# Kernel optimization log

Hardware: AMD Instinct MI355X
Metric: run time of the kernel (lower is better)

Reference implementation:

```python
import jax, jax.numpy as jnp
import numpy as np

B, S, D, H = 8, 1024, 768, 12
DH = D // H
EPS = 1e-5


def setup_inputs() -> dict:
    key = jax.random.key(0)
    ks = jax.random.split(key, 12)
    sc_h = 1.0 / np.sqrt(DH)
    sc_d = 1.0 / np.sqrt(D)
    return {
        "x": jax.random.normal(ks[0], (B, S, D), jnp.float32),
        "ln1_g": jnp.ones((D,), jnp.float32),
        "ln1_b": jnp.zeros((D,), jnp.float32),
        "Wq": jax.random.normal(ks[1], (H, DH, DH), jnp.float32) * sc_h,
        "bq": jax.random.normal(ks[2], (H, DH), jnp.float32) * 0.01,
        "Wk": jax.random.normal(ks[3], (H, DH, DH), jnp.float32) * sc_h,
        "bk": jax.random.normal(ks[4], (H, DH), jnp.float32) * 0.01,
        "Wv": jax.random.normal(ks[5], (H, DH, DH), jnp.float32) * sc_h,
        "bv": jax.random.normal(ks[6], (H, DH), jnp.float32) * 0.01,
        "ln2_g": jnp.ones((D,), jnp.float32),
        "ln2_b": jnp.zeros((D,), jnp.float32),
        "W1": jax.random.normal(ks[7], (D, 4 * D), jnp.float32) * sc_d,  # c_fc (bias=False)
        "W2": jax.random.normal(ks[8], (4 * D, D), jnp.float32) * (1.0 / np.sqrt(4 * D)),  # c_proj (bias=False)
    }


def _layernorm(x, g, b):
    m = jnp.mean(x, axis=-1, keepdims=True)
    v = jnp.mean(jnp.square(x - m), axis=-1, keepdims=True)
    return (x - m) * jax.lax.rsqrt(v + EPS) * g + b


def _msa(x, Wq, bq, Wk, bk, Wv, bv):
    b, s, d = x.shape
    h = x.reshape(b, s, H, DH)  # per-head slices of the embedding
    q = jnp.einsum('bshd,hde->bhse', h, Wq) + bq[None, :, None, :]
    k = jnp.einsum('bshd,hde->bhse', h, Wk) + bk[None, :, None, :]
    v = jnp.einsum('bshd,hde->bhse', h, Wv) + bv[None, :, None, :]
    scores = jnp.einsum('bhse,bhte->bhst', q, k) / np.sqrt(DH).astype(np.float32)
    attn = jax.nn.softmax(scores, axis=-1)
    o = jnp.einsum('bhst,bhte->bhse', attn, v)
    return o.transpose(0, 2, 1, 3).reshape(b, s, d)  # concat heads


def reference(x, ln1_g, ln1_b, Wq, bq, Wk, bk, Wv, bv, ln2_g, ln2_b, W1, W2):
    out = x + _msa(_layernorm(x, ln1_g, ln1_b), Wq, bq, Wk, bk, Wv, bv)
    h = _layernorm(out, ln2_g, ln2_b)
    ffn = jnp.dot(jax.nn.gelu(jnp.dot(h, W1), approximate=False), W2)
    return out + ffn
```

## Files before the change

kernel.cpp:

```cpp
#include <hip/hip_runtime.h>
#include <hip/hip_bf16.h>
#include <math.h>

#define B_ 8
#define S_ 1024
#define D_ 768
#define H_ 12
#define QSCALE 0.18033688011112042f

typedef __attribute__((ext_vector_type(8))) short short8;
typedef __attribute__((ext_vector_type(4))) float floatx4;
typedef unsigned short ushort_t;

__device__ __forceinline__ ushort_t f2bf(float f) {
  unsigned int u = __builtin_bit_cast(unsigned int, f);
  u += 0x7fffu + ((u >> 16) & 1u);
  return (ushort_t)(u >> 16);
}

__device__ __forceinline__ unsigned int pkbf(float a, float b) {
  __hip_bfloat162 h = __float22bfloat162_rn(make_float2(a, b));
  unsigned int r;
  __builtin_memcpy(&r, &h, sizeof(r));
  return r;
}

__device__ __forceinline__ float gelu_f(float x) {
  const float z = fabsf(x) * 0.70710678118654752f;
  const float t = __builtin_amdgcn_rcpf(1.0f + 0.3275911f * z);
  const float p =
      t * (0.254829592f +
           t * (-0.284496736f +
                t * (1.421413741f + t * (-1.453152027f + t * 1.061405429f))));
  const float e = __expf(-z * z);
  const float erfv = 1.0f - p * e;
  return 0.5f * x * (1.0f + copysignf(erfv, x));
}

template <int N>
__device__ __forceinline__ void wait_vmcnt() {
  if constexpr (N == 0)
    asm volatile("s_waitcnt vmcnt(0)" ::: "memory");
  else if constexpr (N == 6)
    asm volatile("s_waitcnt vmcnt(6)" ::: "memory");
  else
    asm volatile("s_waitcnt vmcnt(8)" ::: "memory");
}

__global__ __launch_bounds__(256) void ln_bf16(
    const float* __restrict__ in, const float* __restrict__ g,
    const float* __restrict__ bias, ushort_t* __restrict__ out) {
  const int row = blockIdx.x * 4 + (threadIdx.x >> 6);
  const int lane = threadIdx.x & 63;
  const float* p = in + (size_t)row * D_;
  float4 v[3];
#pragma unroll
  for (int j = 0; j < 3; ++j) v[j] = *(const float4*)(p + j * 256 + lane * 4);
  float s = 0.f;
#pragma unroll
  for (int j = 0; j < 3; ++j) s += (v[j].x + v[j].y) + (v[j].z + v[j].w);
#pragma unroll
  for (int m = 1; m < 64; m <<= 1) s += __shfl_xor(s, m);
  const float mean = s * (1.0f / D_);
  float q = 0.f;
#pragma unroll
  for (int j = 0; j < 3; ++j) {
    const float a = v[j].x - mean, b = v[j].y - mean;
    const float c = v[j].z - mean, d = v[j].w - mean;
    q += (a * a + b * b) + (c * c + d * d);
  }
#pragma unroll
  for (int m = 1; m < 64; m <<= 1) q += __shfl_xor(q, m);
  const float rstd = rsqrtf(q * (1.0f / D_) + 1e-5f);
  ushort_t* o = out + (size_t)row * D_;
#pragma unroll
  for (int j = 0; j < 3; ++j) {
    const float4 gv = *(const float4*)(g + j * 256 + lane * 4);
    const float4 bv = *(const float4*)(bias + j * 256 + lane * 4);
    const unsigned int p01 = pkbf((v[j].x - mean) * rstd * gv.x + bv.x,
                                  (v[j].y - mean) * rstd * gv.y + bv.y);
    const unsigned int p23 = pkbf((v[j].z - mean) * rstd * gv.z + bv.z,
                                  (v[j].w - mean) * rstd * gv.w + bv.w);
    *(uint2*)(o + j * 256 + lane * 4) = make_uint2(p01, p23);
  }
}

__global__ __launch_bounds__(256) void transpose_cast(
    const float* __restrict__ W, ushort_t* __restrict__ Wt, int Kdim, int Ndim) {
  __shared__ float tile[32][33];
  const int n0 = blockIdx.x * 32, k0 = blockIdx.y * 32;
  const int tx = threadIdx.x & 31, ty = threadIdx.x >> 5;
#pragma unroll
  for (int i = 0; i < 32; i += 8)
    tile[ty + i][tx] = W[(size_t)(k0 + ty + i) * Ndim + n0 + tx];
  __syncthreads();
#pragma unroll
  for (int i = 0; i < 32; i += 8)
    Wt[(size_t)(n0 + ty + i) * Kdim + k0 + tx] = f2bf(tile[tx][ty + i]);
}

__global__ __launch_bounds__(256) void trans_w64(
    const float* __restrict__ Wq, const float* __restrict__ Wk,
    const float* __restrict__ Wv, ushort_t* __restrict__ Wqt,
    ushort_t* __restrict__ Wkt, ushort_t* __restrict__ Wvt) {
  const int h = blockIdx.x;
  const float* W = blockIdx.y == 0 ? Wq : blockIdx.y == 1 ? Wk : Wv;
  ushort_t* O = blockIdx.y == 0 ? Wqt : blockIdx.y == 1 ? Wkt : Wvt;
  __shared__ float t[64][65];
  const int tid = threadIdx.x;
#pragma unroll
  for (int i = 0; i < 16; ++i) {
    const int idx = tid + i * 256;
    t[idx >> 6][idx & 63] = W[h * 4096 + idx];
  }
  __syncthreads();
#pragma unroll
  for (int i = 0; i < 16; ++i) {
    const int idx = tid + i * 256;
    O[h * 4096 + idx] = f2bf(t[idx & 63][idx >> 6]);
  }
}

__global__ __launch_bounds__(256) void qkv_mfma(
    const ushort_t* __restrict__ xbf,
    const ushort_t* __restrict__ Wqt, const ushort_t* __restrict__ Wkt,
    const ushort_t* __restrict__ Wvt,
    const float* __restrict__ bq, const float* __restrict__ bk,
    const float* __restrict__ bv,
    ushort_t* __restrict__ qo, ushort_t* __restrict__ ko,
    ushort_t* __restrict__ vt) {
  const int h = blockIdx.y;
  const int mb = blockIdx.x * 128;
  const int tid = threadIdx.x;
  const int wave = tid >> 6, lane = tid & 63;
  const int lc = lane & 15, kq = lane >> 4;
  const int wm = wave * 32;

  short8 af[2][2];
#pragma unroll
  for (int mi = 0; mi < 2; ++mi)
#pragma unroll
    for (int kc = 0; kc < 2; ++kc)
      af[mi][kc] = *(const short8*)(xbf + (size_t)(mb + wm + mi * 16 + lc) * D_ +
                                    h * 64 + kc * 32 + kq * 8);

  const ushort_t* Wp[3] = {Wqt + h * 4096, Wkt + h * 4096, Wvt + h * 4096};
  floatx4 acc[3][2][4] = {};
#pragma unroll
  for (int w3 = 0; w3 < 3; ++w3)
#pragma unroll
    for (int n = 0; n < 4; ++n)
#pragma unroll
      for (int kc = 0; kc < 2; ++kc) {
        const short8 bfv =
            *(const short8*)(Wp[w3] + (n * 16 + lc) * 64 + kc * 32 + kq * 8);
#pragma unroll
        for (int mi = 0; mi < 2; ++mi)
          acc[w3][mi][n] = __builtin_amdgcn_mfma_f32_16x16x32_bf16(
              af[mi][kc], bfv, acc[w3][mi][n], 0, 0, 0);
      }

  const int b = mb >> 10;
  const size_t obase = (size_t)(b * H_ + h) * (S_ * 64);
#pragma unroll
  for (int w3 = 0; w3 < 2; ++w3) {
    const float* bias = (w3 == 0 ? bq : bk) + h * 64;
    ushort_t* outp = w3 == 0 ? qo : ko;
#pragma unroll
    for (int n = 0; n < 4; ++n) {
      const int e = n * 16 + lc;
      const float bvv = bias[e];
#pragma unroll
      for (int mi = 0; mi < 2; ++mi)
#pragma unroll
        for (int r = 0; r < 4; ++r) {
          const int sl = (mb & 1023) + wm + mi * 16 + kq * 4 + r;
          float v = acc[w3][mi][n][r] + bvv;
          if (w3 == 0) v *= QSCALE;
          outp[obase + (size_t)sl * 64 + e] = f2bf(v);
        }
    }
  }
#pragma unroll
  for (int n = 0; n < 4; ++n) {
    const int e = n * 16 + lc;
    const float bvv = bv[h * 64 + e];
#pragma unroll
    for (int mi = 0; mi < 2; ++mi) {
      const int sl0 = (mb & 1023) + wm + mi * 16 + kq * 4;
      const unsigned int p01 =
          pkbf(acc[2][mi][n][0] + bvv, acc[2][mi][n][1] + bvv);
      const unsigned int p23 =
          pkbf(acc[2][mi][n][2] + bvv, acc[2][mi][n][3] + bvv);
      *(uint2*)(vt + obase + (size_t)e * S_ + sl0) = make_uint2(p01, p23);
    }
  }
}

__global__ __launch_bounds__(256) void attn_mfma(
    const ushort_t* __restrict__ qb, const ushort_t* __restrict__ kb,
    const ushort_t* __restrict__ vt, const float* __restrict__ x,
    float* __restrict__ out1) {
  const int bh = blockIdx.x;
  const int tid = threadIdx.x;
  const int wave = tid >> 6, lane = tid & 63;
  const int lc = lane & 15, kq = lane >> 4;
  const int q0 = blockIdx.y * 128 + wave * 32;

  __shared__ __align__(16) ushort_t Ks[64 * 64];
  __shared__ __align__(16) ushort_t Vs[64 * 64];
  __shared__ __align__(16) ushort_t Pw[4][2][16 * 72];

  const ushort_t* qp = qb + (size_t)bh * (S_ * 64);
  const ushort_t* kp = kb + (size_t)bh * (S_ * 64);
  const ushort_t* vp = vt + (size_t)bh * (S_ * 64);

  short8 qf[2][2];
#pragma unroll
  for (int qi = 0; qi < 2; ++qi)
#pragma unroll
    for (int kc = 0; kc < 2; ++kc)
      qf[qi][kc] = *(const short8*)(qp + (size_t)(q0 + qi * 16 + lc) * 64 +
                                    kc * 32 + kq * 8);

  const int srow = tid >> 3;
  const int sgc = ((tid & 7) ^ (srow & 7)) * 8;
  const int slds = srow * 64 + (tid & 7) * 8;
  const int swz = lc & 7;

  float l_r[2] = {0.0f, 0.0f};
  floatx4 oacc[2][4] = {};

  for (int kt = 0; kt < 16; ++kt) {
#pragma unroll
    for (int half = 0; half < 2; ++half) {
      const int r = half * 32 + srow;
      __builtin_amdgcn_global_load_lds(
          (const __attribute__((address_space(1))) unsigned int*)
              (kp + (size_t)(kt * 64 + r) * 64 + sgc),
          (__attribute__((address_space(3))) unsigned int*)
              (Ks + half * 2048 + slds), 16, 0, 0);
      __builtin_amdgcn_global_load_lds(
          (const __attribute__((address_space(1))) unsigned int*)
              (vp + (size_t)r * S_ + kt * 64 + sgc),
          (__attribute__((address_space(3))) unsigned int*)
              (Vs + half * 2048 + slds), 16, 0, 0);
    }
    __syncthreads();

    floatx4 sacc[2][4] = {};
#pragma unroll
    for (int mi = 0; mi < 4; ++mi) {
      const int row = (mi * 16 + lc) * 64;
#pragma unroll
      for (int kc = 0; kc < 2; ++kc) {
        const short8 kf =
            *(const short8*)(Ks + row + ((kc * 4 + kq) ^ swz) * 8);
        sacc[0][mi] = __builtin_amdgcn_mfma_f32_16x16x32_bf16(
            kf, qf[0][kc], sacc[0][mi], 0, 0, 0);
        sacc[1][mi] = __builtin_amdgcn_mfma_f32_16x16x32_bf16(
            kf, qf[1][kc], sacc[1][mi], 0, 0, 0);
      }
    }

#pragma unroll
    for (int qi = 0; qi < 2; ++qi) {
      float pr[4][4];
      float sm = 0.f;
#pragma unroll
      for (int mi = 0; mi < 4; ++mi)
#pragma unroll
        for (int r = 0; r < 4; ++r) {
          pr[mi][r] = exp2f(sacc[qi][mi][r]);
          sm += pr[mi][r];
        }
      l_r[qi] += sm;
#pragma unroll
      for (int mi = 0; mi < 4; ++mi) {
        const unsigned int p01 = pkbf(pr[mi][0], pr[mi][1]);
        const unsigned int p23 = pkbf(pr[mi][2], pr[mi][3]);
        *(uint2*)(&Pw[wave][qi][lc * 72 + mi * 16 + kq * 4]) =
            make_uint2(p01, p23);
      }
    }
    asm volatile("s_waitcnt lgkmcnt(0)" ::: "memory");

    short8 pf[2][2];
#pragma unroll
    for (int qi = 0; qi < 2; ++qi)
#pragma unroll
      for (int kc = 0; kc < 2; ++kc)
        pf[qi][kc] =
            *(const short8*)(&Pw[wave][qi][lc * 72 + kc * 32 + kq * 8]);
#pragma unroll
    for (int mi = 0; mi < 4; ++mi) {
      const int row = (mi * 16 + lc) * 64;
#pragma unroll
      for (int kc = 0; kc < 2; ++kc) {
        const short8 vf =
            *(const short8*)(Vs + row + ((kc * 4 + kq) ^ swz) * 8);
        oacc[0][mi] = __builtin_amdgcn_mfma_f32_16x16x32_bf16(
            vf, pf[0][kc], oacc[0][mi], 0, 0, 0);
        oacc[1][mi] = __builtin_amdgcn_mfma_f32_16x16x32_bf16(
            vf, pf[1][kc], oacc[1][mi], 0, 0, 0);
      }
    }
    __syncthreads();
  }

  const int b = bh / H_, h = bh % H_;
  float* Ow = (float*)&Pw[wave][0][0];
#pragma unroll
  for (int qi = 0; qi < 2; ++qi) {
    float lt = l_r[qi];
    lt += __shfl_xor(lt, 16);
    lt += __shfl_xor(lt, 32);
    const float inv = 1.0f / lt;
#pragma unroll
    for (int mi = 0; mi < 4; ++mi) {
      floatx4 ov = oacc[qi][mi];
      ov[0] *= inv; ov[1] *= inv; ov[2] *= inv; ov[3] *= inv;
      *(floatx4*)(&Ow[lc * 68 + mi * 16 + kq * 4]) = ov;
    }
    asm volatile("s_waitcnt lgkmcnt(0)" ::: "memory");
    const int row = (lane >> 3) & 7, c8 = (lane & 7) * 4;
#pragma unroll
    for (int rg = 0; rg < 2; ++rg) {
      const int qq = rg * 8 + row;
      const size_t gbase =
          ((size_t)(b * S_) + q0 + qi * 16 + qq) * D_ + h * 64 + c8;
#pragma unroll
      for (int j = 0; j < 2; ++j) {
        const float4 ov = *(const float4*)(&Ow[qq * 68 + j * 32 + c8]);
        const float4 xv = *(const float4*)(x + gbase + j * 32);
        *(float4*)(out1 + gbase + j * 32) =
            make_float4(ov.x + xv.x, ov.y + xv.y, ov.z + xv.z, ov.w + xv.w);
      }
    }
    asm volatile("s_waitcnt lgkmcnt(0)" ::: "memory");
  }
}

template <int BM, int BN, int N, int K, bool GELU, bool RESID, bool OUT_BF16,
          bool XCDMAP>
__global__ __launch_bounds__(256) void gemm_pipe(
    const ushort_t* __restrict__ A, const ushort_t* __restrict__ Bt,
    const float* __restrict__ resid, void* __restrict__ Cout) {
  constexpr int MI = BM / 32;
  constexpr int NJ = BN / 32;
  constexpr int LPT = (BM + BN) / 32;
  constexpr int NT = K / 64;

  int mb, nb;
  if constexpr (XCDMAP) {
    const int lin = blockIdx.x;
    const int xcd = lin & 7, slot = lin >> 3;
    const int mbg = slot / (N / 128), nbi = slot - mbg * (N / 128);
    mb = (xcd * 16 + mbg) * 64;
    nb = nbi * 128;
  } else {
    nb = blockIdx.x * BN;
    mb = blockIdx.y * BM;
  }

  const int tid = threadIdx.x;
  const int wave = tid >> 6, lane = tid & 63;
  const int wm = (wave >> 1) * (BM / 2), wn = (wave & 1) * (BN / 2);

  __shared__ __align__(16) ushort_t Asp[2][BM * 64];
  __shared__ __align__(16) ushort_t Bsp[2][BN * 64];

  const int sr = tid >> 3;
  const int sc8 = (tid & 7) * 8;
  const int sgx = ((tid & 7) ^ (sr & 7)) * 8;

  auto stage = [&](int t, int buf) {
    const int kb = t * 64;
#pragma unroll
    for (int j = 0; j < BM / 32; ++j) {
      const int row = j * 32 + sr;
      __builtin_amdgcn_global_load_lds(
          (const __attribute__((address_space(1))) unsigned int*)
              (A + (size_t)(mb + row) * K + kb + sgx),
          (__attribute__((address_space(3))) unsigned int*)
              (&Asp[buf][row * 64 + sc8]), 16, 0, 0);
    }
#pragma unroll
    for (int j = 0; j < BN / 32; ++j) {
      const int row = j * 32 + sr;
      __builtin_amdgcn_global_load_lds(
          (const __attribute__((address_space(1))) unsigned int*)
              (Bt + (size_t)(nb + row) * K + kb + sgx),
          (__attribute__((address_space(3))) unsigned int*)
              (&Bsp[buf][row * 64 + sc8]), 16, 0, 0);
    }
  };

  stage(0, 0);
  stage(1, 1);
  wait_vmcnt<LPT>();
  __builtin_amdgcn_s_barrier();
  __builtin_amdgcn_sched_barrier(0);

  const int lc = lane & 15, kq = lane >> 4, swz = lc & 7;
  floatx4 acc[MI][NJ] = {};

#pragma unroll 1
  for (int t = 0; t < NT; ++t) {
    const int cur = t & 1;
    short8 af[MI][2], bfr[NJ][2];
#pragma unroll
    for (int i = 0; i < MI; ++i)
#pragma unroll
      for (int ks = 0; ks < 2; ++ks)
        af[i][ks] = *(const short8*)(&Asp[cur][(wm + i * 16 + lc) * 64 +
                                               ((ks * 4 + kq) ^ swz) * 8]);
#pragma unroll
    for (int j = 0; j < NJ; ++j)
#pragma unroll
      for (int ks = 0; ks < 2; ++ks)
        bfr[j][ks] = *(const short8*)(&Bsp[cur][(wn + j * 16 + lc) * 64 +
                                                ((ks * 4 + kq) ^ swz) * 8]);
    asm volatile("s_waitcnt lgkmcnt(0)" ::: "memory");
    __builtin_amdgcn_sched_barrier(0);
    __builtin_amdgcn_s_barrier();
    __builtin_amdgcn_sched_barrier(0);
    if (t + 2 < NT) stage(t + 2, cur);
    __builtin_amdgcn_sched_barrier(0);
    __builtin_amdgcn_s_setprio(1);
#pragma unroll
    for (int ks = 0; ks < 2; ++ks)
#pragma unroll
      for (int i = 0; i < MI; ++i)
#pragma unroll
        for (int j = 0; j < NJ; ++j)
          acc[i][j] = __builtin_amdgcn_mfma_f32_16x16x32_bf16(
              af[i][ks], bfr[j][ks], acc[i][j], 0, 0, 0);
    __builtin_amdgcn_s_setprio(0);
    if (t + 2 < NT)
      wait_vmcnt<LPT>();
    else if (t + 1 < NT)
      wait_vmcnt<0>();
    if (t + 1 < NT) {
      __builtin_amdgcn_s_barrier();
      __builtin_amdgcn_sched_barrier(0);
    }
  }

  const int lcol = lane & 15, lr4 = (lane >> 4) * 4;
#pragma unroll
  for (int i = 0; i < MI; ++i)
#pragma unroll
    for (int r = 0; r < 4; ++r) {
      const int m = mb + wm + i * 16 + lr4 + r;
#pragma unroll
      for (int j = 0; j < NJ; ++j) {
        const int col = nb + wn + j * 16 + lcol;
        float vv = acc[i][j][r];
        if (GELU) vv = gelu_f(vv);
        if (RESID) vv += resid[(size_t)m * N + col];
        if (OUT_BF16)
          ((ushort_t*)Cout)[(size_t)m * N + col] = f2bf(vv);
        else
          ((float*)Cout)[(size_t)m * N + col] = vv;
      }
    }
}

extern "C" void kernel_launch(void* const* d_in, const int* in_sizes, int n_in,
                              void* d_out, int out_size, void* d_ws, size_t ws_size,
                              hipStream_t stream) {
  (void)in_sizes; (void)n_in; (void)out_size; (void)ws_size;
  const float* x     = (const float*)d_in[0];
  const float* ln1_g = (const float*)d_in[1];
  const float* ln1_b = (const float*)d_in[2];
  const float* Wq    = (const float*)d_in[3];
  const float* bq    = (const float*)d_in[4];
  const float* Wk    = (const float*)d_in[5];
  const float* bk    = (const float*)d_in[6];
  const float* Wv    = (const float*)d_in[7];
  const float* bv    = (const float*)d_in[8];
  const float* ln2_g = (const float*)d_in[9];
  const float* ln2_b = (const float*)d_in[10];
  const float* W1    = (const float*)d_in[11];
  const float* W2    = (const float*)d_in[12];
  float* out = (float*)d_out;

  const size_t n = (size_t)B_ * S_ * D_;
  ushort_t* u = (ushort_t*)d_ws;
  ushort_t* xbf  = u;
  ushort_t* qb   = xbf + n;
  ushort_t* kb   = qb + n;
  ushort_t* vt   = kb + n;
  ushort_t* xbf2 = vt + n;
  ushort_t* act  = xbf2 + n;
  ushort_t* Wt1  = act + (size_t)8192 * 3072;
  ushort_t* Wt2  = Wt1 + (size_t)3072 * 768;
  ushort_t* Wqt  = Wt2 + (size_t)768 * 3072;
  ushort_t* Wkt  = Wqt + H_ * 4096;
  ushort_t* Wvt  = Wkt + H_ * 4096;
  float* out1 = (float*)(Wvt + H_ * 4096);

  trans_w64<<<dim3(12, 3), dim3(256), 0, stream>>>(Wq, Wk, Wv, Wqt, Wkt, Wvt);
  transpose_cast<<<dim3(96, 24), dim3(256), 0, stream>>>(W1, Wt1, 768, 3072);
  transpose_cast<<<dim3(24, 96), dim3(256), 0, stream>>>(W2, Wt2, 3072, 768);
  ln_bf16<<<dim3(2048), dim3(256), 0, stream>>>(x, ln1_g, ln1_b, xbf);
  qkv_mfma<<<dim3(64, 12), dim3(256), 0, stream>>>(xbf, Wqt, Wkt, Wvt,
                                                   bq, bk, bv, qb, kb, vt);
  attn_mfma<<<dim3(96, 8), dim3(256), 0, stream>>>(qb, kb, vt, x, out1);
  ln_bf16<<<dim3(2048), dim3(256), 0, stream>>>(out1, ln2_g, ln2_b, xbf2);
  gemm_pipe<128, 128, 3072, 768, true, false, true, false>
      <<<dim3(24, 64), dim3(256), 0, stream>>>(xbf2, Wt1, nullptr, act);
  gemm_pipe<64, 128, 768, 3072, false, true, false, true>
      <<<dim3(768), dim3(256), 0, stream>>>(act, Wt2, out1, out);
}
```

Baseline: 292.9 us.

## Double-buffer K/V tiles in attention kernel to overlap loads with MFMA

The attention kernel now keeps two LDS buffers for K and V and prefetches the next key tile with global_load_lds while the current tile is processed. Partial vmcnt waits and raw s_barrier calls replace the full __syncthreads, so that global load latency can hide behind the QK and PV MFMA work. This doubles the K/V LDS footprint, which may lower occupancy, and depends on the vmcnt count matching the four loads issued per tile.

```diff
diff --git a/kernel.cpp b/kernel.cpp
--- a/kernel.cpp
+++ b/kernel.cpp
@@ -41,6 +41,8 @@
 __device__ __forceinline__ void wait_vmcnt() {
   if constexpr (N == 0)
     asm volatile("s_waitcnt vmcnt(0)" ::: "memory");
+  else if constexpr (N == 4)
+    asm volatile("s_waitcnt vmcnt(4)" ::: "memory");
   else if constexpr (N == 6)
     asm volatile("s_waitcnt vmcnt(6)" ::: "memory");
   else
@@ -207,8 +209,8 @@
   const int lc = lane & 15, kq = lane >> 4;
   const int q0 = blockIdx.y * 128 + wave * 32;
 
-  __shared__ __align__(16) ushort_t Ks[64 * 64];
-  __shared__ __align__(16) ushort_t Vs[64 * 64];
+  __shared__ __align__(16) ushort_t Ks[2][64 * 64];
+  __shared__ __align__(16) ushort_t Vs[2][64 * 64];
   __shared__ __align__(16) ushort_t Pw[4][2][16 * 72];
 
   const ushort_t* qp = qb + (size_t)bh * (S_ * 64);
@@ -228,10 +230,7 @@
   const int slds = srow * 64 + (tid & 7) * 8;
   const int swz = lc & 7;
 
-  float l_r[2] = {0.0f, 0.0f};
-  floatx4 oacc[2][4] = {};
-
-  for (int kt = 0; kt < 16; ++kt) {
+  auto stageKV = [&](int kt, int buf) {
 #pragma unroll
     for (int half = 0; half < 2; ++half) {
       const int r = half * 32 + srow;
@@ -239,14 +238,31 @@
           (const __attribute__((address_space(1))) unsigned int*)
               (kp + (size_t)(kt * 64 + r) * 64 + sgc),
           (__attribute__((address_space(3))) unsigned int*)
-              (Ks + half * 2048 + slds), 16, 0, 0);
+              (&Ks[buf][half * 2048 + slds]), 16, 0, 0);
       __builtin_amdgcn_global_load_lds(
           (const __attribute__((address_space(1))) unsigned int*)
               (vp + (size_t)r * S_ + kt * 64 + sgc),
           (__attribute__((address_space(3))) unsigned int*)
-              (Vs + half * 2048 + slds), 16, 0, 0);
-    }
-    __syncthreads();
+              (&Vs[buf][half * 2048 + slds]), 16, 0, 0);
+    }
+  };
+
+  float l_r[2] = {0.0f, 0.0f};
+  floatx4 oacc[2][4] = {};
+
+  stageKV(0, 0);
+
+#pragma unroll 1
+  for (int kt = 0; kt < 16; ++kt) {
+    const int cur = kt & 1;
+    if (kt + 1 < 16) stageKV(kt + 1, cur ^ 1);
+    if (kt + 1 < 16)
+      wait_vmcnt<4>();
+    else
+      wait_vmcnt<0>();
+    __builtin_amdgcn_sched_barrier(0);
+    __builtin_amdgcn_s_barrier();
+    __builtin_amdgcn_sched_barrier(0);
 
     floatx4 sacc[2][4] = {};
 #pragma unroll
@@ -255,7 +271,7 @@
 #pragma unroll
       for (int kc = 0; kc < 2; ++kc) {
         const short8 kf =
-            *(const short8*)(Ks + row + ((kc * 4 + kq) ^ swz) * 8);
+            *(const short8*)(&Ks[cur][row + ((kc * 4 + kq) ^ swz) * 8]);
         sacc[0][mi] = __builtin_amdgcn_mfma_f32_16x16x32_bf16(
             kf, qf[0][kc], sacc[0][mi], 0, 0, 0);
         sacc[1][mi] = __builtin_amdgcn_mfma_f32_16x16x32_bf16(
@@ -298,14 +314,18 @@
 #pragma unroll
       for (int kc = 0; kc < 2; ++kc) {
         const short8 vf =
-            *(const short8*)(Vs + row + ((kc * 4 + kq) ^ swz) * 8);
+            *(const short8*)(&Vs[cur][row + ((kc * 4 + kq) ^ swz) * 8]);
         oacc[0][mi] = __builtin_amdgcn_mfma_f32_16x16x32_bf16(
             vf, pf[0][kc], oacc[0][mi], 0, 0, 0);
         oacc[1][mi] = __builtin_amdgcn_mfma_f32_16x16x32_bf16(
             vf, pf[1][kc], oacc[1][mi], 0, 0, 0);
       }
     }
-    __syncthreads();
+    if (kt + 1 < 16) {
+      __builtin_amdgcn_sched_barrier(0);
+      __builtin_amdgcn_s_barrier();
+      __builtin_amdgcn_sched_barrier(0);
+    }
   }
 
   const int b = bh / H_, h = bh % H_;
```

Result: no change. 289.5 us (-1.2%).
